# Optimization experiments

Hardware: AMD Instinct MI355X
Metric: run time of the kernel (lower is better)

Reference implementation:

```python
import jax, jax.numpy as jnp
import numpy as np

D_MODEL = 1024
NUM_HEADS = 16


def setup_inputs() -> dict:
    key = jax.random.key(0)
    ks = jax.random.split(key, 5)
    B, S, D = 2, 2048, D_MODEL
    scale = 1.0 / np.sqrt(D)
    return {
        "x": jax.random.normal(ks[0], (B, S, D), dtype=jnp.float32),
        "q_proj_weight": jax.random.normal(ks[1], (D, D), dtype=jnp.float32) * scale,
        "k_proj_weight": jax.random.normal(ks[2], (D, D), dtype=jnp.float32) * scale,
        "v_proj_weight": jax.random.normal(ks[3], (D, D), dtype=jnp.float32) * scale,
        "o_proj_weight": jax.random.normal(ks[4], (D, D), dtype=jnp.float32) * scale,
    }


def _attn(x, qw, kw, vw, ow, num_heads):
    B, S, D = x.shape
    d_k = D // num_heads
    q = x @ qw.T  # [B,S,D]
    k = x @ kw.T
    v = x @ vw.T
    # split heads: [B, H, S, d_k]
    q = q.reshape(B, S, num_heads, d_k).transpose(0, 2, 1, 3)
    k = k.reshape(B, S, num_heads, d_k).transpose(0, 2, 1, 3)
    v = v.reshape(B, S, num_heads, d_k).transpose(0, 2, 1, 3)
    scores = jnp.einsum('bhqd,bhkd->bhqk', q, k) / jnp.sqrt(jnp.asarray(d_k, x.dtype))
    causal = jnp.tril(jnp.ones((S, S), dtype=bool))  # [S,S]
    scores = jnp.where(causal[None, None], scores, jnp.asarray(-jnp.inf, x.dtype))
    attn = jax.nn.softmax(scores, axis=-1)
    out = jnp.einsum('bhqk,bhkd->bhqd', attn, v)  # [B,H,S,d_k]
    out = out.transpose(0, 2, 1, 3).reshape(B, S, D)
    return out @ ow.T


def reference(x, q_proj_weight, k_proj_weight, v_proj_weight, o_proj_weight):
    return _attn(x, q_proj_weight, k_proj_weight, v_proj_weight, o_proj_weight, NUM_HEADS)
```

## Files before the change

kernel.cpp:

```cpp
#include <hip/hip_runtime.h>

typedef __attribute__((ext_vector_type(8))) short short8;
typedef __attribute__((ext_vector_type(4))) float f32x4;

#define MFMA(a,b,c) __builtin_amdgcn_mfma_f32_16x16x32_bf16((a),(b),(c),0,0,0)

#define B_  2
#define S_  2048
#define D_  1024
#define H_  16
#define DK  64
#define KDIM 1024

typedef unsigned int u32;
typedef __attribute__((address_space(1))) const u32 gu32;
typedef __attribute__((address_space(3))) u32 lu32;

__device__ __forceinline__ void gll16(const unsigned short* g, unsigned short* l){
  __builtin_amdgcn_global_load_lds((gu32*)g, (lu32*)l, 16, 0, 0);
}

__device__ __forceinline__ unsigned short f2bf(float f){
  unsigned int u = __float_as_uint(f);
  u += 0x7fffu + ((u >> 16) & 1u);
  return (unsigned short)(u >> 16);
}

__device__ __forceinline__ u32 pkbf(float lo, float hi){
  u32 a = __float_as_uint(lo) + 0x8000u;
  u32 b = __float_as_uint(hi) + 0x8000u;
  return __builtin_amdgcn_perm(b, a, 0x07060302u);
}

__global__ void cvt_all(const float* __restrict__ x,  const float* __restrict__ qw,
                        const float* __restrict__ kw, const float* __restrict__ vw,
                        const float* __restrict__ ow,
                        unsigned short* __restrict__ xb,  unsigned short* __restrict__ wqb,
                        unsigned short* __restrict__ wkb, unsigned short* __restrict__ wvb,
                        unsigned short* __restrict__ wob,
                        int n4x, int n4w){
  int i = blockIdx.x * 256 + threadIdx.x;
  const float* src; unsigned short* dst; int n4;
  switch (blockIdx.y) {
    case 0:  src = x;  dst = xb;  n4 = n4x; break;
    case 1:  src = qw; dst = wqb; n4 = n4w; break;
    case 2:  src = kw; dst = wkb; n4 = n4w; break;
    case 3:  src = vw; dst = wvb; n4 = n4w; break;
    default: src = ow; dst = wob; n4 = n4w; break;
  }
  if (i >= n4) return;
  float4 f = reinterpret_cast<const float4*>(src)[i];
  ushort4 u;
  u.x = f2bf(f.x); u.y = f2bf(f.y); u.z = f2bf(f.z); u.w = f2bf(f.w);
  reinterpret_cast<ushort4*>(dst)[i] = u;
}

struct FragsQKV { short8 a0[4], a1[4], b0[3][2], b1[3][2]; };

__global__ __launch_bounds__(256, 2) void gemm_qkv(
    const unsigned short* __restrict__ X,
    const unsigned short* __restrict__ Wq,
    const unsigned short* __restrict__ Wk,
    const unsigned short* __restrict__ Wv,
    unsigned short* __restrict__ Qo,
    unsigned short* __restrict__ Ko,
    unsigned short* __restrict__ Vo)
{
  const int n0 = blockIdx.x * 64;
  const int m0 = blockIdx.y * 128;

  __shared__ unsigned short As[2][128 * 64];
  __shared__ unsigned short Bs[2][3][64 * 64];

  const int tid  = threadIdx.x;
  const int wid  = tid >> 6, lane = tid & 63;
  const int wm   = (wid >> 1) * 64, wn = (wid & 1) * 32;
  const int lr   = lane & 15, c = lane >> 4;
  const int sw   = lr & 7;
  const int pc0  = (c ^ sw) * 8;
  const int pc1  = ((c ^ 4) ^ sw) * 8;

  const int srow = lane >> 3;
  const int scol = ((lane & 7) ^ srow) * 8;
  const unsigned short* gA  = X  + (size_t)(m0 + wid * 32 + srow) * KDIM + scol;
  const unsigned short* gBq = Wq + (size_t)(n0 + wid * 16 + srow) * KDIM + scol;
  const unsigned short* gBk = Wk + (size_t)(n0 + wid * 16 + srow) * KDIM + scol;
  const unsigned short* gBv = Wv + (size_t)(n0 + wid * 16 + srow) * KDIM + scol;

  auto stage = [&](int buf, int k0) {
    unsigned short* la  = &As[buf][(wid * 32) * 64];
    unsigned short* lbq = &Bs[buf][0][(wid * 16) * 64];
    unsigned short* lbk = &Bs[buf][1][(wid * 16) * 64];
    unsigned short* lbv = &Bs[buf][2][(wid * 16) * 64];
#pragma unroll
    for (int i = 0; i < 4; i++) gll16(gA + (size_t)(i * 8) * KDIM + k0, la + i * 512);
#pragma unroll
    for (int i = 0; i < 2; i++) gll16(gBq + (size_t)(i * 8) * KDIM + k0, lbq + i * 512);
#pragma unroll
    for (int i = 0; i < 2; i++) gll16(gBk + (size_t)(i * 8) * KDIM + k0, lbk + i * 512);
#pragma unroll
    for (int i = 0; i < 2; i++) gll16(gBv + (size_t)(i * 8) * KDIM + k0, lbv + i * 512);
  };

  auto ldfr = [&](int buf, FragsQKV& f) {
    const unsigned short* AS = As[buf];
#pragma unroll
    for (int i = 0; i < 4; i++) {
      f.a0[i] = *(const short8*)&AS[(wm + i * 16 + lr) * 64 + pc0];
      f.a1[i] = *(const short8*)&AS[(wm + i * 16 + lr) * 64 + pc1];
    }
#pragma unroll
    for (int z = 0; z < 3; z++) {
      const unsigned short* BS = Bs[buf][z];
#pragma unroll
      for (int j = 0; j < 2; j++) {
        f.b0[z][j] = *(const short8*)&BS[(wn + j * 16 + lr) * 64 + pc0];
        f.b1[z][j] = *(const short8*)&BS[(wn + j * 16 + lr) * 64 + pc1];
      }
    }
  };

  f32x4 acc[3][4][2];
  const f32x4 z4 = {0.f, 0.f, 0.f, 0.f};
#pragma unroll
  for (int z = 0; z < 3; z++)
    for (int i = 0; i < 4; i++)
      for (int j = 0; j < 2; j++) acc[z][i][j] = z4;

  auto mfmas = [&](const FragsQKV& f) {
#pragma unroll
    for (int z = 0; z < 3; z++) {
      if (z == 2) {
#pragma unroll
        for (int i = 0; i < 4; i++)
#pragma unroll
          for (int j = 0; j < 2; j++) {
            acc[z][i][j] = MFMA(f.b0[z][j], f.a0[i], acc[z][i][j]);
            acc[z][i][j] = MFMA(f.b1[z][j], f.a1[i], acc[z][i][j]);
          }
      } else {
#pragma unroll
        for (int i = 0; i < 4; i++)
#pragma unroll
          for (int j = 0; j < 2; j++) {
            acc[z][i][j] = MFMA(f.a0[i], f.b0[z][j], acc[z][i][j]);
            acc[z][i][j] = MFMA(f.a1[i], f.b1[z][j], acc[z][i][j]);
          }
      }
    }
  };

  stage(0, 0);
  stage(1, 64);

  FragsQKV f;
  const int NT = KDIM / 64;
  for (int t = 0; t < NT - 2; ++t) {
    const int buf = t & 1;
    asm volatile("s_waitcnt vmcnt(10)" ::: "memory");
    __builtin_amdgcn_s_barrier();
    asm volatile("" ::: "memory");
    ldfr(buf, f);
    asm volatile("s_waitcnt lgkmcnt(0)" ::: "memory");
    __builtin_amdgcn_sched_barrier(0);
    __builtin_amdgcn_s_barrier();
    asm volatile("" ::: "memory");
    stage(buf, (t + 2) * 64);
    __builtin_amdgcn_sched_barrier(0);
    mfmas(f);
  }
  asm volatile("s_waitcnt vmcnt(10)" ::: "memory");
  __builtin_amdgcn_s_barrier();
  asm volatile("" ::: "memory");
  ldfr((NT - 2) & 1, f);
  mfmas(f);
  asm volatile("s_waitcnt vmcnt(0)" ::: "memory");
  __builtin_amdgcn_s_barrier();
  asm volatile("" ::: "memory");
  ldfr((NT - 1) & 1, f);
  mfmas(f);

  const int rbase = (lane >> 4) * 4;
  for (int i = 0; i < 4; i++)
    for (int j = 0; j < 2; j++)
      for (int r = 0; r < 4; r++) {
        int m = m0 + wm + i * 16 + rbase + r;
        int n = n0 + wn + j * 16 + lr;
        int bb = m >> 11, s = m & 2047, h = n >> 6, d = n & 63;
        float vq = acc[0][i][j][r] * 0.18033688f;
        Qo[(((bb * H_ + h) * S_) + s) * DK + d] = f2bf(vq);
        Ko[(((bb * H_ + h) * S_) + s) * DK + d] = f2bf(acc[1][i][j][r]);
      }
  for (int i = 0; i < 4; i++)
    for (int j = 0; j < 2; j++)
      for (int r = 0; r < 4; r++) {
        int dfull = n0 + wn + j * 16 + rbase + r;
        int sfull = m0 + wm + i * 16 + lr;
        int h = dfull >> 6, d = dfull & 63;
        int bb = sfull >> 11, s = sfull & 2047;
        Vo[(((bb * H_ + h) * DK) + d) * S_ + s] = f2bf(acc[2][i][j][r]);
      }
}

__global__ __launch_bounds__(512, 4) void attn(
    const unsigned short* __restrict__ Q,
    const unsigned short* __restrict__ K,
    const unsigned short* __restrict__ V,
    unsigned short* __restrict__ O)
{
  const int h = blockIdx.y, b = blockIdx.z;
  const int qt = b ? (15 - blockIdx.x) : blockIdx.x;

  const unsigned short* __restrict__ Qh = Q + (size_t)((b * H_ + h) * S_) * DK;
  const unsigned short* __restrict__ Kh = K + (size_t)((b * H_ + h) * S_) * DK;
  const unsigned short* __restrict__ Vh = V + (size_t)((b * H_ + h) * DK) * S_;

  __shared__ unsigned short Ks[3][64 * 64];
  __shared__ unsigned short Vs[3][64 * 64];
  __shared__ unsigned short Ps[8][16][72];

  const int tid = threadIdx.x, wid = tid >> 6, lane = tid & 63;
  const int lr = lane & 15;
  const int row4 = (lane >> 4) * 4;
  const int q0 = qt * 128;
  const int qcol = q0 + wid * 16 + lr;
  const int qwmin = q0 + wid * 16;
  const int qwmax = qwmin + 15;
  const int lk = (lane >> 4) * 8;

  const int pc0 = (((lane >> 4) + lr) & 7) * 8;
  const int pc1 = (((lane >> 4) + 4 + lr) & 7) * 8;

  const int sr8 = lane >> 3;
  const int sc8 = lane & 7;
  const int sg  = (sc8 - sr8) & 7;
  const int stRow = wid * 8 + sr8;
  const unsigned short* gK = Kh + (size_t)stRow * DK + sg * 8;
  const unsigned short* gV = Vh + (size_t)stRow * S_ + sg * 8;
  unsigned short* kd[3] = {&Ks[0][wid * 8 * 64], &Ks[1][wid * 8 * 64], &Ks[2][wid * 8 * 64]};
  unsigned short* vd[3] = {&Vs[0][wid * 8 * 64], &Vs[1][wid * 8 * 64], &Vs[2][wid * 8 * 64]};

  const short ONE = (short)0x3F80;
  const short8 ones = {ONE, ONE, ONE, ONE, ONE, ONE, ONE, ONE};

  short8 qf[2];
  qf[0] = *(const short8*)&Qh[(q0 + wid * 16 + lr) * DK + lk];
  qf[1] = *(const short8*)&Qh[(q0 + wid * 16 + lr) * DK + 32 + lk];

  const f32x4 z4 = {0.f, 0.f, 0.f, 0.f};
  f32x4 o[4];
  for (int i = 0; i < 4; i++) o[i] = z4;
  f32x4 rs = z4;

  auto tile = [&](int k0, const unsigned short* KS, const unsigned short* VS){
    if (k0 > qwmax) return;
    f32x4 sc[4];
    __builtin_amdgcn_s_setprio(1);
    for (int nt = 0; nt < 4; nt++) {
      short8 kb0 = *(const short8*)&KS[(nt * 16 + lr) * 64 + pc0];
      short8 kb1 = *(const short8*)&KS[(nt * 16 + lr) * 64 + pc1];
      f32x4 s = MFMA(kb0, qf[0], z4);
      sc[nt] = MFMA(kb1, qf[1], s);
    }
    __builtin_amdgcn_s_setprio(0);
    if (k0 + 63 > qwmin) {
      for (int nt = 0; nt < 4; nt++) {
        int kg = k0 + nt * 16 + row4;
        for (int r = 0; r < 4; r++)
          if (kg + r > qcol) sc[nt][r] = -INFINITY;
      }
    }
    for (int nt = 0; nt < 4; nt++) {
      float p0 = __builtin_amdgcn_exp2f(sc[nt][0]);
      float p1 = __builtin_amdgcn_exp2f(sc[nt][1]);
      float p2 = __builtin_amdgcn_exp2f(sc[nt][2]);
      float p3 = __builtin_amdgcn_exp2f(sc[nt][3]);
      uint2 pk;
      pk.x = pkbf(p0, p1);
      pk.y = pkbf(p2, p3);
      *(uint2*)&Ps[wid][lr][nt * 16 + row4] = pk;
    }
    short8 pf0 = *(const short8*)&Ps[wid][lr][lk];
    short8 pf1 = *(const short8*)&Ps[wid][lr][32 + lk];
    __builtin_amdgcn_s_setprio(1);
    rs = MFMA(ones, pf0, rs);
    rs = MFMA(ones, pf1, rs);
    for (int dt = 0; dt < 4; dt++) {
      short8 vb0 = *(const short8*)&VS[(dt * 16 + lr) * 64 + pc0];
      short8 vb1 = *(const short8*)&VS[(dt * 16 + lr) * 64 + pc1];
      o[dt] = MFMA(vb0, pf0, o[dt]);
      o[dt] = MFMA(vb1, pf1, o[dt]);
    }
    __builtin_amdgcn_s_setprio(0);
  };

  const int T = 2 * qt + 2;

  gll16(gK,                     kd[0]);
  gll16(gV,                     vd[0]);
  gll16(gK + (size_t)64 * DK,   kd[1]);
  gll16(gV + 64,                vd[1]);

  for (int t = 0; t < T; ++t) {
    if (t < T - 1) asm volatile("s_waitcnt vmcnt(2)" ::: "memory");
    else           asm volatile("s_waitcnt vmcnt(0)" ::: "memory");
    __builtin_amdgcn_s_barrier();
    asm volatile("" ::: "memory");
    if (t + 2 < T) {
      const int cbuf = (t + 2) % 3;
      gll16(gK + (size_t)((t + 2) * 64) * DK, kd[cbuf]);
      gll16(gV + (t + 2) * 64,                vd[cbuf]);
    }
    tile(t * 64, &Ks[t % 3][0], &Vs[t % 3][0]);
  }

  const float inv = 1.0f / rs[0];

  const int srow = q0 + wid * 16 + lr;
  for (int dt = 0; dt < 4; dt++) {
    uint2 pk;
    pk.x = pkbf(o[dt][0] * inv, o[dt][1] * inv);
    pk.y = pkbf(o[dt][2] * inv, o[dt][3] * inv);
    *(uint2*)&O[(size_t)(b * S_ + srow) * D_ + h * DK + dt * 16 + row4] = pk;
  }
}

struct Frags { short8 a0[4], a1[4], b0[2], b1[2]; };

__global__ __launch_bounds__(256) void gemm_oproj(
    const unsigned short* __restrict__ A,
    const unsigned short* __restrict__ W,
    float* __restrict__ out)
{
  const int n0 = blockIdx.x * 64;
  const int m0 = blockIdx.y * 128;

  __shared__ unsigned short As[2][128 * 64];
  __shared__ unsigned short Bs[2][64 * 64];

  const int tid  = threadIdx.x;
  const int wid  = tid >> 6, lane = tid & 63;
  const int wm   = (wid >> 1) * 64, wn = (wid & 1) * 32;
  const int lr   = lane & 15, c = lane >> 4;
  const int sw   = lr & 7;
  const int pc0  = (c ^ sw) * 8;
  const int pc1  = ((c ^ 4) ^ sw) * 8;

  const int srow = lane >> 3;
  const int scol = ((lane & 7) ^ srow) * 8;
  const unsigned short* gA = A + (size_t)(m0 + wid * 32 + srow) * KDIM + scol;
  const unsigned short* gB = W + (size_t)(n0 + wid * 16 + srow) * KDIM + scol;

  auto stage = [&](int buf, int k0) {
    unsigned short* la = &As[buf][(wid * 32) * 64];
    unsigned short* lb = &Bs[buf][(wid * 16) * 64];
#pragma unroll
    for (int i = 0; i < 4; i++) gll16(gA + (size_t)(i * 8) * KDIM + k0, la + i * 512);
#pragma unroll
    for (int i = 0; i < 2; i++) gll16(gB + (size_t)(i * 8) * KDIM + k0, lb + i * 512);
  };

  auto ldfr = [&](int buf, Frags& f) {
    const unsigned short* AS = As[buf];
    const unsigned short* BS = Bs[buf];
#pragma unroll
    for (int i = 0; i < 4; i++) {
      f.a0[i] = *(const short8*)&AS[(wm + i * 16 + lr) * 64 + pc0];
      f.a1[i] = *(const short8*)&AS[(wm + i * 16 + lr) * 64 + pc1];
    }
#pragma unroll
    for (int j = 0; j < 2; j++) {
      f.b0[j] = *(const short8*)&BS[(wn + j * 16 + lr) * 64 + pc0];
      f.b1[j] = *(const short8*)&BS[(wn + j * 16 + lr) * 64 + pc1];
    }
  };

  f32x4 acc[4][2];
  const f32x4 z4 = {0.f, 0.f, 0.f, 0.f};
  for (int i = 0; i < 4; i++)
    for (int j = 0; j < 2; j++) acc[i][j] = z4;

  auto mfmas = [&](const Frags& f) {
#pragma unroll
    for (int i = 0; i < 4; i++)
#pragma unroll
      for (int j = 0; j < 2; j++) {
        acc[i][j] = MFMA(f.a0[i], f.b0[j], acc[i][j]);
        acc[i][j] = MFMA(f.a1[i], f.b1[j], acc[i][j]);
      }
  };

  stage(0, 0);
  stage(1, 64);

  Frags f;
  const int NT = KDIM / 64;
  for (int t = 0; t < NT - 2; ++t) {
    const int buf = t & 1;
    asm volatile("s_waitcnt vmcnt(6)" ::: "memory");
    __builtin_amdgcn_s_barrier();
    asm volatile("" ::: "memory");
    ldfr(buf, f);
    asm volatile("s_waitcnt lgkmcnt(0)" ::: "memory");
    __builtin_amdgcn_sched_barrier(0);
    __builtin_amdgcn_s_barrier();
    asm volatile("" ::: "memory");
    stage(buf, (t + 2) * 64);
    __builtin_amdgcn_sched_barrier(0);
    mfmas(f);
  }
  asm volatile("s_waitcnt vmcnt(6)" ::: "memory");
  __builtin_amdgcn_s_barrier();
  asm volatile("" ::: "memory");
  ldfr((NT - 2) & 1, f);
  mfmas(f);
  asm volatile("s_waitcnt vmcnt(0)" ::: "memory");
  __builtin_amdgcn_s_barrier();
  asm volatile("" ::: "memory");
  ldfr((NT - 1) & 1, f);
  mfmas(f);

  const int rbase = (lane >> 4) * 4;
  for (int i = 0; i < 4; i++)
    for (int j = 0; j < 2; j++)
      for (int r = 0; r < 4; r++) {
        int m = m0 + wm + i * 16 + rbase + r;
        int n = n0 + wn + j * 16 + lr;
        out[(size_t)m * D_ + n] = acc[i][j][r];
      }
}

extern "C" void kernel_launch(void* const* d_in, const int* in_sizes, int n_in,
                              void* d_out, int out_size, void* d_ws, size_t ws_size,
                              hipStream_t stream) {
  const float* x  = (const float*)d_in[0];
  const float* qw = (const float*)d_in[1];
  const float* kw = (const float*)d_in[2];
  const float* vw = (const float*)d_in[3];
  const float* ow = (const float*)d_in[4];
  float* out = (float*)d_out;

  char* ws = (char*)d_ws;
  size_t off = 0;
  auto alloc = [&](size_t bytes) -> void* {
    void* p = ws + off;
    off += (bytes + 255) & ~(size_t)255;
    return p;
  };
  const size_t XN = (size_t)B_ * S_ * D_;
  const size_t WN = (size_t)D_ * D_;
  unsigned short* xb  = (unsigned short*)alloc(XN * 2);
  unsigned short* wqb = (unsigned short*)alloc(WN * 2);
  unsigned short* wkb = (unsigned short*)alloc(WN * 2);
  unsigned short* wvb = (unsigned short*)alloc(WN * 2);
  unsigned short* wob = (unsigned short*)alloc(WN * 2);
  unsigned short* Qb  = (unsigned short*)alloc(XN * 2);
  unsigned short* Kb  = (unsigned short*)alloc(XN * 2);
  unsigned short* Vb  = (unsigned short*)alloc(XN * 2);
  unsigned short* Ob  = (unsigned short*)alloc(XN * 2);

  cvt_all<<<dim3((XN / 4 + 255) / 256, 5), dim3(256), 0, stream>>>(
      x, qw, kw, vw, ow, xb, wqb, wkb, wvb, wob, (int)(XN / 4), (int)(WN / 4));

  gemm_qkv<<<dim3(D_ / 64, (B_ * S_) / 128), dim3(256), 0, stream>>>(
      xb, wqb, wkb, wvb, Qb, Kb, Vb);

  attn<<<dim3(S_ / 128, H_, B_), dim3(512), 0, stream>>>(Qb, Kb, Vb, Ob);

  gemm_oproj<<<dim3(D_ / 64, (B_ * S_) / 128), dim3(256), 0, stream>>>(Ob, wob, out);
}
```

Measured before the change: 161.4 us.

## Keep attention probabilities in registers with permuted K layout and 128-key tiles

```diff
diff --git a/kernel.cpp b/kernel.cpp
--- a/kernel.cpp
+++ b/kernel.cpp
@@ -2,6 +2,7 @@
 
 typedef __attribute__((ext_vector_type(8))) short short8;
 typedef __attribute__((ext_vector_type(4))) float f32x4;
+typedef __attribute__((ext_vector_type(4))) unsigned int u32x4;
 
 #define MFMA(a,b,c) __builtin_amdgcn_mfma_f32_16x16x32_bf16((a),(b),(c),0,0,0)
 
@@ -215,30 +216,38 @@
   const unsigned short* __restrict__ Kh = K + (size_t)((b * H_ + h) * S_) * DK;
   const unsigned short* __restrict__ Vh = V + (size_t)((b * H_ + h) * DK) * S_;
 
-  __shared__ unsigned short Ks[3][64 * 64];
-  __shared__ unsigned short Vs[3][64 * 64];
-  __shared__ unsigned short Ps[8][16][72];
+  __shared__ unsigned short Ks0[128 * 64];
+  __shared__ unsigned short Ks1[128 * 64];
+  __shared__ unsigned short Vs0[64 * 128];
+  __shared__ unsigned short Vs1[64 * 128];
 
   const int tid = threadIdx.x, wid = tid >> 6, lane = tid & 63;
-  const int lr = lane & 15;
-  const int row4 = (lane >> 4) * 4;
+  const int lr = lane & 15, c = lane >> 4;
+  const int row4 = c * 4;
   const int q0 = qt * 128;
   const int qcol = q0 + wid * 16 + lr;
-  const int qwmin = q0 + wid * 16;
-  const int qwmax = qwmin + 15;
-  const int lk = (lane >> 4) * 8;
-
-  const int pc0 = (((lane >> 4) + lr) & 7) * 8;
-  const int pc1 = (((lane >> 4) + 4 + lr) & 7) * 8;
+  const int lk = c * 8;
+
+  const int s8 = (lr & 3) + 2 * (lr >> 2);
+  const int pcA = ((c + s8) & 7) * 8;
+  const int pcB = ((c + s8 + 4) & 7) * 8;
+  const int rowb = (8 * (lr >> 2) + (lr & 3)) * 64;
+  int pcV[4];
+#pragma unroll
+  for (int j = 0; j < 4; j++) pcV[j] = ((4 * j + c + lr) & 15) * 8;
 
   const int sr8 = lane >> 3;
   const int sc8 = lane & 7;
-  const int sg  = (sc8 - sr8) & 7;
-  const int stRow = wid * 8 + sr8;
-  const unsigned short* gK = Kh + (size_t)stRow * DK + sg * 8;
-  const unsigned short* gV = Vh + (size_t)stRow * S_ + sg * 8;
-  unsigned short* kd[3] = {&Ks[0][wid * 8 * 64], &Ks[1][wid * 8 * 64], &Ks[2][wid * 8 * 64]};
-  unsigned short* vd[3] = {&Vs[0][wid * 8 * 64], &Vs[1][wid * 8 * 64], &Vs[2][wid * 8 * 64]};
+  const int sgK1 = (sc8 - sr8 - 2 * ((2 * wid) & 3)) & 7;
+  const int sgK2 = (sc8 - sr8 - 2 * ((2 * wid + 1) & 3)) & 7;
+  const unsigned short* gK1 = Kh + (size_t)(16 * wid + sr8) * DK + sgK1 * 8;
+  const unsigned short* gK2 = Kh + (size_t)(16 * wid + 8 + sr8) * DK + sgK2 * 8;
+  const int vr = lane >> 4;
+  const int vc16 = lane & 15;
+  const int sgV1 = (vc16 - (8 * wid + vr)) & 15;
+  const int sgV2 = (sgV1 - 4) & 15;
+  const unsigned short* gV1 = Vh + (size_t)(8 * wid + vr) * S_ + sgV1 * 8;
+  const unsigned short* gV2 = Vh + (size_t)(8 * wid + 4 + vr) * S_ + sgV2 * 8;
 
   const short ONE = (short)0x3F80;
   const short8 ones = {ONE, ONE, ONE, ONE, ONE, ONE, ONE, ONE};
@@ -252,66 +261,71 @@
   for (int i = 0; i < 4; i++) o[i] = z4;
   f32x4 rs = z4;
 
-  auto tile = [&](int k0, const unsigned short* KS, const unsigned short* VS){
-    if (k0 > qwmax) return;
-    f32x4 sc[4];
+  auto stage = [&](int par, int k0) {
+    unsigned short* lk_ = (par ? Ks1 : Ks0) + (wid * 16) * 64;
+    unsigned short* lv_ = (par ? Vs1 : Vs0) + (wid * 8) * 128;
+    gll16(gK1 + (size_t)k0 * DK, lk_);
+    gll16(gK2 + (size_t)k0 * DK, lk_ + 512);
+    gll16(gV1 + k0, lv_);
+    gll16(gV2 + k0, lv_ + 512);
+  };
+
+  auto tile = [&](int k0, const unsigned short* KS, const unsigned short* VS,
+                  bool diag) {
+    short8 pf[4];
+#pragma unroll
+    for (int j = 0; j < 4; j++) {
+      const int ro = rowb + j * 2048;
+      short8 kb;
+      __builtin_amdgcn_s_setprio(1);
+      kb = *(const short8*)&KS[ro + pcA];
+      f32x4 ta = MFMA(kb, qf[0], z4);
+      kb = *(const short8*)&KS[ro + pcB];
+      f32x4 sa = MFMA(kb, qf[1], ta);
+      kb = *(const short8*)&KS[ro + 256 + pcB];
+      f32x4 tb = MFMA(kb, qf[0], z4);
+      kb = *(const short8*)&KS[ro + 256 + pcA];
+      f32x4 sb = MFMA(kb, qf[1], tb);
+      __builtin_amdgcn_s_setprio(0);
+      if (diag) {
+        const int kg = k0 + 8 * c + 32 * j;
+#pragma unroll
+        for (int r = 0; r < 4; r++) {
+          if (kg + r > qcol)     sa[r] = -INFINITY;
+          if (kg + 4 + r > qcol) sb[r] = -INFINITY;
+        }
+      }
+      u32 w0 = pkbf(__builtin_amdgcn_exp2f(sa[0]), __builtin_amdgcn_exp2f(sa[1]));
+      u32 w1 = pkbf(__builtin_amdgcn_exp2f(sa[2]), __builtin_amdgcn_exp2f(sa[3]));
+      u32 w2 = pkbf(__builtin_amdgcn_exp2f(sb[0]), __builtin_amdgcn_exp2f(sb[1]));
+      u32 w3 = pkbf(__builtin_amdgcn_exp2f(sb[2]), __builtin_amdgcn_exp2f(sb[3]));
+      u32x4 a = {w0, w1, w2, w3};
+      pf[j] = *(short8*)&a;
+    }
     __builtin_amdgcn_s_setprio(1);
-    for (int nt = 0; nt < 4; nt++) {
-      short8 kb0 = *(const short8*)&KS[(nt * 16 + lr) * 64 + pc0];
-      short8 kb1 = *(const short8*)&KS[(nt * 16 + lr) * 64 + pc1];
-      f32x4 s = MFMA(kb0, qf[0], z4);
-      sc[nt] = MFMA(kb1, qf[1], s);
+    rs = MFMA(ones, pf[0], rs);
+    rs = MFMA(ones, pf[1], rs);
+    rs = MFMA(ones, pf[2], rs);
+    rs = MFMA(ones, pf[3], rs);
+#pragma unroll
+    for (int dt = 0; dt < 4; dt++) {
+      const int rb2 = (dt * 16 + lr) * 128;
+#pragma unroll
+      for (int j = 0; j < 4; j++) {
+        short8 vb = *(const short8*)&VS[rb2 + pcV[j]];
+        o[dt] = MFMA(vb, pf[j], o[dt]);
+      }
     }
     __builtin_amdgcn_s_setprio(0);
-    if (k0 + 63 > qwmin) {
-      for (int nt = 0; nt < 4; nt++) {
-        int kg = k0 + nt * 16 + row4;
-        for (int r = 0; r < 4; r++)
-          if (kg + r > qcol) sc[nt][r] = -INFINITY;
-      }
-    }
-    for (int nt = 0; nt < 4; nt++) {
-      float p0 = __builtin_amdgcn_exp2f(sc[nt][0]);
-      float p1 = __builtin_amdgcn_exp2f(sc[nt][1]);
-      float p2 = __builtin_amdgcn_exp2f(sc[nt][2]);
-      float p3 = __builtin_amdgcn_exp2f(sc[nt][3]);
-      uint2 pk;
-      pk.x = pkbf(p0, p1);
-      pk.y = pkbf(p2, p3);
-      *(uint2*)&Ps[wid][lr][nt * 16 + row4] = pk;
-    }
-    short8 pf0 = *(const short8*)&Ps[wid][lr][lk];
-    short8 pf1 = *(const short8*)&Ps[wid][lr][32 + lk];
-    __builtin_amdgcn_s_setprio(1);
-    rs = MFMA(ones, pf0, rs);
-    rs = MFMA(ones, pf1, rs);
-    for (int dt = 0; dt < 4; dt++) {
-      short8 vb0 = *(const short8*)&VS[(dt * 16 + lr) * 64 + pc0];
-      short8 vb1 = *(const short8*)&VS[(dt * 16 + lr) * 64 + pc1];
-      o[dt] = MFMA(vb0, pf0, o[dt]);
-      o[dt] = MFMA(vb1, pf1, o[dt]);
-    }
-    __builtin_amdgcn_s_setprio(0);
-  };
-
-  const int T = 2 * qt + 2;
-
-  gll16(gK,                     kd[0]);
-  gll16(gV,                     vd[0]);
-  gll16(gK + (size_t)64 * DK,   kd[1]);
-  gll16(gV + 64,                vd[1]);
-
+  };
+
+  const int T = qt + 1;
+
+  stage(0, 0);
   for (int t = 0; t < T; ++t) {
-    if (t < T - 1) asm volatile("s_waitcnt vmcnt(2)" ::: "memory");
-    else           asm volatile("s_waitcnt vmcnt(0)" ::: "memory");
-    __builtin_amdgcn_s_barrier();
-    asm volatile("" ::: "memory");
-    if (t + 2 < T) {
-      const int cbuf = (t + 2) % 3;
-      gll16(gK + (size_t)((t + 2) * 64) * DK, kd[cbuf]);
-      gll16(gV + (t + 2) * 64,                vd[cbuf]);
-    }
-    tile(t * 64, &Ks[t % 3][0], &Vs[t % 3][0]);
+    __syncthreads();
+    if (t + 1 < T) stage((t + 1) & 1, (t + 1) * 128);
+    tile(t * 128, (t & 1) ? Ks1 : Ks0, (t & 1) ? Vs1 : Vs0, t == T - 1);
   }
 
   const float inv = 1.0f / rs[0];
```

New measurement: 153.3 us. 1.05x faster.
